# Performance work log

Hardware: AMD Instinct MI355X
Metric: run time of the kernel (lower is better)

## Reference

```python
import jax, jax.numpy as jnp
import numpy as np

B, N, D, H, S = 2, 1024, 1024, 16, 4
DH = D // H  # dim_head = 64


def setup_inputs() -> dict:
    key = jax.random.key(0)
    ks = jax.random.split(key, 7)
    w = lambda k, shape: jax.random.normal(k, shape, dtype=jnp.float32) * 0.02
    return {
        "x": jax.random.normal(ks[0], (B, N, D), dtype=jnp.float32),
        "Wq": w(ks[1], (S, D, D)),
        "Wk": w(ks[2], (S, D, D)),
        "Wv": w(ks[3], (S, D, D)),
        "Wg": w(ks[4], (S, D)),
        "bg": jnp.zeros((S,), jnp.float32),
        "Wo": w(ks[5], (D, D)),
        "bo": jnp.zeros((D,), jnp.float32),
        "hyp_w": jnp.ones((S,), jnp.float32),
        "temperature": jnp.float32(1.0),
    }


def reference(x, Wq, Wk, Wv, Wg, bg, Wo, bo, hyp_w, temperature):
    # Training branch of EnhancedUncertaintyAttention, all S samples batched.
    b, n, d = x.shape
    scale = DH ** -0.5
    temp = jnp.clip(temperature, 0.1, 10.0)

    # coherence gate on mean-pooled tokens: [b, S]
    coh = jax.nn.sigmoid(x.mean(axis=1) @ Wg.T + bg)

    def proj(W):  # torch Linear: x @ W.T ; W: [S, out, in] -> [s,b,h,n,dh]
        y = jnp.einsum('bnd,sed->sbne', x, W)
        return y.reshape(S, b, n, H, DH).transpose(0, 1, 3, 2, 4)

    q, k, v = proj(Wq), proj(Wk), proj(Wv)

    dots = jnp.einsum('sbhid,sbhjd->sbhij', q, k) * scale
    attn = jax.nn.softmax(dots / temp, axis=-1)            # [S,b,h,n,n]
    out = jnp.einsum('sbhij,sbhjd->sbhid', attn, v)        # [S,b,h,n,dh]
    out = out.transpose(0, 1, 3, 2, 4).reshape(S, b, n, d) # [S,b,n,d]
    out = out * coh.T[:, :, None, None]                    # per-sample gate

    gw = jax.nn.softmax(hyp_w / temp)                      # hypothesis weights [S]
    combined = jnp.einsum('s,sbnd->bnd', gw, out)
    combined_attn = jnp.einsum('s,sbhij->bhij', gw, attn)

    y = combined @ Wo.T + bo  # to_out; dropout p treated as 0 (deterministic)
    return y, combined_attn.mean(axis=1)
```

## Files before the change

kernel.cpp:

```cpp
#include <hip/hip_runtime.h>
#include <hip/hip_bf16.h>

typedef __attribute__((ext_vector_type(8))) short s16x8;
typedef __attribute__((ext_vector_type(4))) float f32x4;

#define MAT2M 2097152
#define NPAD 72
#define PPAD 72

__device__ __forceinline__ unsigned short f2bf(float f) {
  union { float f; unsigned u; } c; c.f = f;
  unsigned u = c.u;
  unsigned r = (u + 0x7fffu + ((u >> 16) & 1u)) >> 16;
  return (unsigned short)r;
}

__device__ __forceinline__ unsigned pk2bf(float a, float b) {
  union { __hip_bfloat162 h; unsigned u; } c;
  c.h = __float22bfloat162_rn(make_float2(a, b));
  return c.u;
}

__device__ __forceinline__ void async16(const unsigned short* g, unsigned short* l) {
  __builtin_amdgcn_global_load_lds(
      (const __attribute__((address_space(1))) unsigned int*)g,
      (__attribute__((address_space(3))) unsigned int*)l, 16, 0, 0);
}

__global__ __launch_bounds__(256) void k_cvt(const float* __restrict__ in,
                                             unsigned short* __restrict__ out, int n) {
  int i = (blockIdx.x * 256 + threadIdx.x) * 4;
  if (i < n) {
    float4 v = *(const float4*)&in[i];
    ushort4 o;
    o.x = f2bf(v.x); o.y = f2bf(v.y); o.z = f2bf(v.z); o.w = f2bf(v.w);
    *(ushort4*)&out[i] = o;
  }
}

__global__ __launch_bounds__(256) void k_meanx(const float* __restrict__ x,
                                               float* __restrict__ meanx) {
  int col = blockIdx.x * 256 + threadIdx.x;
  int b = col >> 10, d = col & 1023;
  int n0 = blockIdx.y * 64;
  float s = 0.f;
  for (int n = 0; n < 64; ++n)
    s += x[(size_t)b * 1048576 + (size_t)(n0 + n) * 1024 + d];
  atomicAdd(&meanx[col], s * (1.f / 1024.f));
}

__global__ __launch_bounds__(256) void k_prep(const float* __restrict__ meanx,
                                              const float* __restrict__ Wg,
                                              const float* __restrict__ bg,
                                              const float* __restrict__ hyp,
                                              const float* __restrict__ temp_p,
                                              float* __restrict__ prep) {
  int tid = threadIdx.x;
  int p = tid >> 5, c = tid & 31;
  int s = p >> 1, b = p & 1;
  float partial = 0.f;
  for (int d = c; d < 1024; d += 32)
    partial += meanx[b * 1024 + d] * Wg[s * 1024 + d];
#pragma unroll
  for (int m = 16; m >= 1; m >>= 1) partial += __shfl_xor(partial, m, 64);
  if (c == 0) {
    float coh = 1.f / (1.f + __expf(-(partial + bg[s])));
    prep[4 + s * 2 + b] = coh;
  }
  if (tid == 0) {
    float t = temp_p[0];
    t = fminf(fmaxf(t, 0.1f), 10.f);
    float it = 1.f / t;
    float e0 = hyp[0] * it, e1 = hyp[1] * it, e2 = hyp[2] * it, e3 = hyp[3] * it;
    float mx = fmaxf(fmaxf(e0, e1), fmaxf(e2, e3));
    float x0 = __expf(e0 - mx), x1 = __expf(e1 - mx), x2 = __expf(e2 - mx), x3 = __expf(e3 - mx);
    float inv = 1.f / (x0 + x1 + x2 + x3);
    prep[0] = x0 * inv; prep[1] = x1 * inv; prep[2] = x2 * inv; prep[3] = x3 * inv;
    prep[12] = 0.125f * it * 1.44269504f;
  }
}

__global__ __launch_bounds__(256) void gemm_qkv(
    const unsigned short* __restrict__ xb,
    const unsigned short* __restrict__ wqb,
    const unsigned short* __restrict__ wkb,
    const unsigned short* __restrict__ wvb,
    const float* __restrict__ prep,
    unsigned short* __restrict__ qk,
    unsigned short* __restrict__ vt) {
  __shared__ __align__(16) unsigned short As[128 * 32];
  __shared__ __align__(16) unsigned short Bs[128 * 32];
  const int tid = threadIdx.x;
  const int wid = tid >> 6, ln = tid & 63, lq = ln >> 4, lc = ln & 15;
  const int wr = wid >> 1, wc = wid & 1;
  const int z = blockIdx.z, proj = z >> 2, s = z & 3;
  const unsigned short* Bmat =
      (proj == 0 ? wqb : (proj == 1 ? wkb : wvb)) + (size_t)s * 1048576;
  const int n0 = blockIdx.x * 128, m0 = blockIdx.y * 128;
  const int srow = wid * 32 + (ln >> 2);
  const int scol = (ln & 3) * 8;
  const int lds0 = wid * 1024 + ln * 8;

  f32x4 acc[4][4];
#pragma unroll
  for (int a = 0; a < 4; ++a)
#pragma unroll
    for (int b4 = 0; b4 < 4; ++b4) acc[a][b4] = (f32x4){0.f, 0.f, 0.f, 0.f};

  for (int kt = 0; kt < 32; ++kt) {
    const int k0 = kt * 32;
    __syncthreads();
    async16(&xb[(size_t)(m0 + srow) * 1024 + k0 + scol], &As[lds0]);
    async16(&xb[(size_t)(m0 + srow + 16) * 1024 + k0 + scol], &As[lds0 + 512]);
    async16(&Bmat[(size_t)(n0 + srow) * 1024 + k0 + scol], &Bs[lds0]);
    async16(&Bmat[(size_t)(n0 + srow + 16) * 1024 + k0 + scol], &Bs[lds0 + 512]);
    __syncthreads();
    s16x8 af[4], bf[4];
#pragma unroll
    for (int a = 0; a < 4; ++a)
      af[a] = *(const s16x8*)&As[(wr * 64 + a * 16 + lc) * 32 + lq * 8];
#pragma unroll
    for (int b4 = 0; b4 < 4; ++b4)
      bf[b4] = *(const s16x8*)&Bs[(wc * 64 + b4 * 16 + lc) * 32 + lq * 8];
#pragma unroll
    for (int a = 0; a < 4; ++a)
#pragma unroll
      for (int b4 = 0; b4 < 4; ++b4)
        acc[a][b4] = __builtin_amdgcn_mfma_f32_16x16x32_bf16(af[a], bf[b4], acc[a][b4], 0, 0, 0);
  }

  const float mulv = (proj == 1) ? prep[12] : 1.0f;
  if (z < 8) {
    unsigned short* C = qk + (size_t)z * MAT2M;
#pragma unroll
    for (int a = 0; a < 4; ++a) {
      int row0 = m0 + wr * 64 + a * 16 + lq * 4;
#pragma unroll
      for (int b4 = 0; b4 < 4; ++b4) {
        int col = n0 + wc * 64 + b4 * 16 + lc;
#pragma unroll
        for (int r = 0; r < 4; ++r)
          C[(size_t)(row0 + r) * 1024 + col] = f2bf(acc[a][b4][r] * mulv);
      }
    }
  } else {
#pragma unroll
    for (int a = 0; a < 4; ++a) {
      int row0 = m0 + wr * 64 + a * 16 + lq * 4;
      int bb = row0 >> 10, ii = row0 & 1023;
#pragma unroll
      for (int b4 = 0; b4 < 4; ++b4) {
        int col = n0 + wc * 64 + b4 * 16 + lc;
        int head = col >> 6, dh = col & 63;
        ushort4 pk;
        pk.x = f2bf(acc[a][b4][0]); pk.y = f2bf(acc[a][b4][1]);
        pk.z = f2bf(acc[a][b4][2]); pk.w = f2bf(acc[a][b4][3]);
        *(ushort4*)&vt[(((size_t)((s * 2 + bb) * 16 + head)) << 16) + dh * 1024 + ii] = pk;
      }
    }
  }
}

__device__ __forceinline__ void stage64(const unsigned short* __restrict__ g,
                                        unsigned short* l, int tid) {
  const int r1 = tid >> 3;
  const int c8 = (tid & 7) * 8;
  *(float4*)&l[r1 * NPAD + c8] = *(const float4*)&g[(size_t)r1 * 1024 + c8];
  *(float4*)&l[(r1 + 32) * NPAD + c8] = *(const float4*)&g[(size_t)(r1 + 32) * 1024 + c8];
}

__global__ __launch_bounds__(256) void att_o(
    const unsigned short* __restrict__ qk,
    const unsigned short* __restrict__ vt,
    float* __restrict__ o_s,
    float* __restrict__ linv_ws) {
  __shared__ __align__(16) unsigned short ks[64 * NPAD];
  __shared__ __align__(16) unsigned short vts[64 * NPAD];
  __shared__ __align__(16) unsigned short PB[8 * 16 * PPAD];

  const int tid = threadIdx.x;
  const int wid = tid >> 6, ln = tid & 63, lq = ln >> 4, lc = ln & 15;
  const int i0 = blockIdx.x * 128;
  const int h = blockIdx.y;
  const int sb = blockIdx.z, s = sb >> 1, b = sb & 1;

  const unsigned short* Qg =
      qk + (size_t)s * MAT2M + (size_t)(b * 1024 + i0 + wid * 32) * 1024 + h * 64;
  const unsigned short* Kg = qk + (size_t)(4 + s) * MAT2M + (size_t)b * 1048576 + h * 64;
  const unsigned short* Vtg = vt + (((size_t)(sb * 16 + h)) << 16);

  s16x8 qf[2][2];
#pragma unroll
  for (int g = 0; g < 2; ++g)
#pragma unroll
    for (int kc = 0; kc < 2; ++kc)
      qf[g][kc] = *(const s16x8*)&Qg[(size_t)(g * 16 + lc) * 1024 + kc * 32 + lq * 8];

  f32x4 oaccT[2][4];
#pragma unroll
  for (int g = 0; g < 2; ++g)
#pragma unroll
    for (int db = 0; db < 4; ++db) oaccT[g][db] = (f32x4){0.f, 0.f, 0.f, 0.f};
  float lsum[2] = {0.f, 0.f};
  unsigned short* PBw = PB + wid * 2 * 16 * PPAD;

  for (int jt = 0; jt < 16; ++jt) {
    __syncthreads();
    stage64(Kg + (size_t)jt * 64 * 1024, ks, tid);
    stage64(Vtg + jt * 64, vts, tid);
    __syncthreads();

    f32x4 st[2][4];
#pragma unroll
    for (int g = 0; g < 2; ++g)
#pragma unroll
      for (int jb = 0; jb < 4; ++jb) st[g][jb] = (f32x4){0.f, 0.f, 0.f, 0.f};
#pragma unroll
    for (int jb = 0; jb < 4; ++jb)
#pragma unroll
      for (int kc = 0; kc < 2; ++kc) {
        s16x8 kf = *(const s16x8*)&ks[(jb * 16 + lc) * NPAD + kc * 32 + lq * 8];
        st[0][jb] = __builtin_amdgcn_mfma_f32_16x16x32_bf16(kf, qf[0][kc], st[0][jb], 0, 0, 0);
        st[1][jb] = __builtin_amdgcn_mfma_f32_16x16x32_bf16(kf, qf[1][kc], st[1][jb], 0, 0, 0);
      }

#pragma unroll
    for (int g = 0; g < 2; ++g)
#pragma unroll
      for (int jb = 0; jb < 4; ++jb) {
        float p0 = __builtin_amdgcn_exp2f(st[g][jb][0]);
        float p1 = __builtin_amdgcn_exp2f(st[g][jb][1]);
        float p2 = __builtin_amdgcn_exp2f(st[g][jb][2]);
        float p3 = __builtin_amdgcn_exp2f(st[g][jb][3]);
        lsum[g] += (p0 + p1) + (p2 + p3);
        uint2 pv;
        pv.x = pk2bf(p0, p1);
        pv.y = pk2bf(p2, p3);
        *(uint2*)&PBw[(g * 16 + lc) * PPAD + jb * 16 + lq * 4] = pv;
      }

#pragma unroll
    for (int kc = 0; kc < 2; ++kc) {
      s16x8 pf0 = *(const s16x8*)&PBw[lc * PPAD + kc * 32 + lq * 8];
      s16x8 pf1 = *(const s16x8*)&PBw[(16 + lc) * PPAD + kc * 32 + lq * 8];
#pragma unroll
      for (int db = 0; db < 4; ++db) {
        s16x8 vf = *(const s16x8*)&vts[(db * 16 + lc) * NPAD + kc * 32 + lq * 8];
        oaccT[0][db] = __builtin_amdgcn_mfma_f32_16x16x32_bf16(vf, pf0, oaccT[0][db], 0, 0, 0);
        oaccT[1][db] = __builtin_amdgcn_mfma_f32_16x16x32_bf16(vf, pf1, oaccT[1][db], 0, 0, 0);
      }
    }
  }

  float invl[2];
#pragma unroll
  for (int g = 0; g < 2; ++g) {
    lsum[g] += __shfl_xor(lsum[g], 16, 64);
    lsum[g] += __shfl_xor(lsum[g], 32, 64);
    invl[g] = 1.f / lsum[g];
  }
  if (lq == 0) {
    int base = (sb * 16 + h) * 1024 + i0 + wid * 32 + lc;
    linv_ws[base] = invl[0];
    linv_ws[base + 16] = invl[1];
  }

#pragma unroll
  for (int g = 0; g < 2; ++g) {
    int i = i0 + wid * 32 + g * 16 + lc;
    float* orow = o_s + (size_t)s * MAT2M + (size_t)(b * 1024 + i) * 1024 + h * 64;
#pragma unroll
    for (int db = 0; db < 4; ++db) {
      f32x4 o = oaccT[g][db] * invl[g];
      *(f32x4*)&orow[db * 16 + lq * 4] = o;
    }
  }
}

__global__ __launch_bounds__(256) void att_p(
    const unsigned short* __restrict__ qk,
    const float* __restrict__ prep,
    const float* __restrict__ linv_ws,
    float* __restrict__ out1) {
  __shared__ __align__(16) unsigned short qs[128 * NPAD];
  __shared__ __align__(16) unsigned short ks[64 * NPAD];
  const int tid = threadIdx.x;
  const int wid = tid >> 6, ln = tid & 63, lq = ln >> 4, lc = ln & 15;
  const int j0 = blockIdx.x * 64;
  const int i0 = blockIdx.y * 128;
  const int b = blockIdx.z;

  f32x4 psum[2][4];
#pragma unroll
  for (int g = 0; g < 2; ++g)
#pragma unroll
    for (int jb = 0; jb < 4; ++jb) psum[g][jb] = (f32x4){0.f, 0.f, 0.f, 0.f};

  for (int s = 0; s < 4; ++s) {
    const float wgt = prep[s] * (1.f / 16.f);
    const unsigned short* Qb = qk + (size_t)s * MAT2M + (size_t)(b * 1024 + i0) * 1024;
    const unsigned short* Kb = qk + (size_t)(4 + s) * MAT2M + (size_t)(b * 1024 + j0) * 1024;
    for (int h = 0; h < 16; ++h) {
      __syncthreads();
      stage64(Qb + h * 64, qs, tid);
      stage64(Qb + (size_t)64 * 1024 + h * 64, qs + 64 * NPAD, tid);
      stage64(Kb + h * 64, ks, tid);
      __syncthreads();
      s16x8 qf[2][2];
#pragma unroll
      for (int g = 0; g < 2; ++g)
#pragma unroll
        for (int kc = 0; kc < 2; ++kc)
          qf[g][kc] = *(const s16x8*)&qs[(wid * 32 + g * 16 + lc) * NPAD + kc * 32 + lq * 8];
      float ilr[2];
#pragma unroll
      for (int g = 0; g < 2; ++g)
        ilr[g] = wgt * linv_ws[((s * 2 + b) * 16 + h) * 1024 + i0 + wid * 32 + g * 16 + lc];
      f32x4 st[2][4];
#pragma unroll
      for (int g = 0; g < 2; ++g)
#pragma unroll
        for (int jb = 0; jb < 4; ++jb) st[g][jb] = (f32x4){0.f, 0.f, 0.f, 0.f};
#pragma unroll
      for (int jb = 0; jb < 4; ++jb)
#pragma unroll
        for (int kc = 0; kc < 2; ++kc) {
          s16x8 kf = *(const s16x8*)&ks[(jb * 16 + lc) * NPAD + kc * 32 + lq * 8];
          st[0][jb] = __builtin_amdgcn_mfma_f32_16x16x32_bf16(kf, qf[0][kc], st[0][jb], 0, 0, 0);
          st[1][jb] = __builtin_amdgcn_mfma_f32_16x16x32_bf16(kf, qf[1][kc], st[1][jb], 0, 0, 0);
        }
#pragma unroll
      for (int g = 0; g < 2; ++g)
#pragma unroll
        for (int jb = 0; jb < 4; ++jb)
#pragma unroll
          for (int r = 0; r < 4; ++r)
            psum[g][jb][r] += __builtin_amdgcn_exp2f(st[g][jb][r]) * ilr[g];
    }
  }
#pragma unroll
  for (int g = 0; g < 2; ++g) {
    int i = i0 + wid * 32 + g * 16 + lc;
    float* row = out1 + (size_t)b * 1048576 + (size_t)i * 1024;
#pragma unroll
    for (int jb = 0; jb < 4; ++jb)
      *(f32x4*)&row[j0 + jb * 16 + lq * 4] = psum[g][jb];
  }
}

__global__ __launch_bounds__(256) void k_combine(const float* __restrict__ o_s,
                                                 const float* __restrict__ prep,
                                                 unsigned short* __restrict__ comb) {
  size_t base = (size_t)(blockIdx.x * 256 + threadIdx.x) * 4;
  int m = (int)(base >> 10);
  int b = m >> 10;
  float w0 = prep[0] * prep[4 + 0 * 2 + b];
  float w1 = prep[1] * prep[4 + 1 * 2 + b];
  float w2 = prep[2] * prep[4 + 2 * 2 + b];
  float w3 = prep[3] * prep[4 + 3 * 2 + b];
  float4 v0 = *(const float4*)&o_s[base];
  float4 v1 = *(const float4*)&o_s[(size_t)MAT2M + base];
  float4 v2 = *(const float4*)&o_s[(size_t)2 * MAT2M + base];
  float4 v3 = *(const float4*)&o_s[(size_t)3 * MAT2M + base];
  float4 a;
  a.x = w0 * v0.x + w1 * v1.x + w2 * v2.x + w3 * v3.x;
  a.y = w0 * v0.y + w1 * v1.y + w2 * v2.y + w3 * v3.y;
  a.z = w0 * v0.z + w1 * v1.z + w2 * v2.z + w3 * v3.z;
  a.w = w0 * v0.w + w1 * v1.w + w2 * v2.w + w3 * v3.w;
  ushort4 o;
  o.x = f2bf(a.x); o.y = f2bf(a.y); o.z = f2bf(a.z); o.w = f2bf(a.w);
  *(ushort4*)&comb[base] = o;
}

__global__ __launch_bounds__(256) void gemm_out(
    const unsigned short* __restrict__ Amat,
    const unsigned short* __restrict__ Bmat,
    const float* __restrict__ bias,
    float* __restrict__ y) {
  __shared__ __align__(16) unsigned short As[128 * 32];
  __shared__ __align__(16) unsigned short Bs[128 * 32];
  const int tid = threadIdx.x;
  const int wid = tid >> 6, ln = tid & 63, lq = ln >> 4, lc = ln & 15;
  const int wr = wid >> 1, wc = wid & 1;
  const int n0 = blockIdx.x * 128, m0 = blockIdx.y * 128;
  const int srow = wid * 32 + (ln >> 2);
  const int scol = (ln & 3) * 8;
  const int lds0 = wid * 1024 + ln * 8;

  f32x4 acc[4][4];
#pragma unroll
  for (int a = 0; a < 4; ++a)
#pragma unroll
    for (int b4 = 0; b4 < 4; ++b4) acc[a][b4] = (f32x4){0.f, 0.f, 0.f, 0.f};

  for (int kt = 0; kt < 32; ++kt) {
    const int k0 = kt * 32;
    __syncthreads();
    async16(&Amat[(size_t)(m0 + srow) * 1024 + k0 + scol], &As[lds0]);
    async16(&Amat[(size_t)(m0 + srow + 16) * 1024 + k0 + scol], &As[lds0 + 512]);
    async16(&Bmat[(size_t)(n0 + srow) * 1024 + k0 + scol], &Bs[lds0]);
    async16(&Bmat[(size_t)(n0 + srow + 16) * 1024 + k0 + scol], &Bs[lds0 + 512]);
    __syncthreads();
    s16x8 af[4], bf[4];
#pragma unroll
    for (int a = 0; a < 4; ++a)
      af[a] = *(const s16x8*)&As[(wr * 64 + a * 16 + lc) * 32 + lq * 8];
#pragma unroll
    for (int b4 = 0; b4 < 4; ++b4)
      bf[b4] = *(const s16x8*)&Bs[(wc * 64 + b4 * 16 + lc) * 32 + lq * 8];
#pragma unroll
    for (int a = 0; a < 4; ++a)
#pragma unroll
      for (int b4 = 0; b4 < 4; ++b4)
        acc[a][b4] = __builtin_amdgcn_mfma_f32_16x16x32_bf16(af[a], bf[b4], acc[a][b4], 0, 0, 0);
  }

#pragma unroll
  for (int a = 0; a < 4; ++a) {
    int row0 = m0 + wr * 64 + a * 16 + lq * 4;
#pragma unroll
    for (int b4 = 0; b4 < 4; ++b4) {
      int col = n0 + wc * 64 + b4 * 16 + lc;
      float bv = bias[col];
#pragma unroll
      for (int r = 0; r < 4; ++r)
        y[(size_t)(row0 + r) * 1024 + col] = acc[a][b4][r] + bv;
    }
  }
}

extern "C" void kernel_launch(void* const* d_in, const int* in_sizes, int n_in,
                              void* d_out, int out_size, void* d_ws, size_t ws_size,
                              hipStream_t stream) {
  const float* x    = (const float*)d_in[0];
  const float* Wq   = (const float*)d_in[1];
  const float* Wk   = (const float*)d_in[2];
  const float* Wv   = (const float*)d_in[3];
  const float* Wg   = (const float*)d_in[4];
  const float* bg   = (const float*)d_in[5];
  const float* Wo   = (const float*)d_in[6];
  const float* bo   = (const float*)d_in[7];
  const float* hyp  = (const float*)d_in[8];
  const float* temp = (const float*)d_in[9];

  float* y = (float*)d_out;
  float* out1 = y + MAT2M;

  char* w = (char*)d_ws;
  size_t off = 0;
  auto alloc = [&](size_t bytes) { void* p = w + off; off += (bytes + 255) & ~(size_t)255; return p; };
  unsigned short* xb   = (unsigned short*)alloc((size_t)MAT2M * 2);
  unsigned short* wqb  = (unsigned short*)alloc((size_t)4 * 1048576 * 2);
  unsigned short* wkb  = (unsigned short*)alloc((size_t)4 * 1048576 * 2);
  unsigned short* wvb  = (unsigned short*)alloc((size_t)4 * 1048576 * 2);
  unsigned short* wob  = (unsigned short*)alloc((size_t)1048576 * 2);
  unsigned short* qk   = (unsigned short*)alloc((size_t)8 * MAT2M * 2);
  unsigned short* vt   = (unsigned short*)alloc((size_t)4 * MAT2M * 2);
  float* o_s   = (float*)alloc((size_t)4 * MAT2M * 4);
  unsigned short* comb = (unsigned short*)alloc((size_t)MAT2M * 2);
  float* linv  = (float*)alloc((size_t)131072 * 4);
  float* meanx = (float*)alloc((size_t)2048 * 4);
  float* prep  = (float*)alloc((size_t)16 * 4);

  k_cvt<<<2048, 256, 0, stream>>>(x, xb, MAT2M);
  k_cvt<<<4096, 256, 0, stream>>>(Wq, wqb, 4 * 1048576);
  k_cvt<<<4096, 256, 0, stream>>>(Wk, wkb, 4 * 1048576);
  k_cvt<<<4096, 256, 0, stream>>>(Wv, wvb, 4 * 1048576);
  k_cvt<<<1024, 256, 0, stream>>>(Wo, wob, 1048576);

  hipMemsetAsync(meanx, 0, 2048 * sizeof(float), stream);
  k_meanx<<<dim3(8, 16), 256, 0, stream>>>(x, meanx);
  k_prep<<<1, 256, 0, stream>>>(meanx, Wg, bg, hyp, temp, prep);

  gemm_qkv<<<dim3(8, 16, 12), 256, 0, stream>>>(xb, wqb, wkb, wvb, prep, qk, vt);

  att_o<<<dim3(8, 16, 8), 256, 0, stream>>>(qk, vt, o_s, linv);
  att_p<<<dim3(16, 8, 2), 256, 0, stream>>>(qk, prep, linv, out1);

  k_combine<<<2048, 256, 0, stream>>>(o_s, prep, comb);
  gemm_out<<<dim3(8, 16, 1), 256, 0, stream>>>(comb, wob, bo, y);
}
```

Before: 373.2 us.

## Widen GEMM K-tiles with swizzled LDS, drop attention LDS staging, split att_p by sample

Both GEMMs now load 64-wide K tiles into an XOR-swizzled LDS layout, which halves the barrier count and avoids bank conflicts. The attention kernels drop their shared-memory staging of K and V and read MFMA fragments straight from global memory. att_p is split across samples (grid z 2→8) for more parallelism, and its partial results are merged with atomics into a pre-zeroed output. The per-sample attention output is stored in bf16 instead of fp32 to halve combine traffic, and the three weight conversions are fused into one launch. The risks are uncoalesced direct global fragment loads, float-atomic contention and ordering nondeterminism in the averaged attention map, and extra bf16 rounding.

New measurement: 539.0 us. 1.44x slower.

```diff
diff --git a/kernel.cpp b/kernel.cpp
--- a/kernel.cpp
+++ b/kernel.cpp
@@ -5,7 +5,6 @@
 typedef __attribute__((ext_vector_type(4))) float f32x4;
 
 #define MAT2M 2097152
-#define NPAD 72
 #define PPAD 72
 
 __device__ __forceinline__ unsigned short f2bf(float f) {
@@ -19,6 +18,10 @@
   union { __hip_bfloat162 h; unsigned u; } c;
   c.h = __float22bfloat162_rn(make_float2(a, b));
   return c.u;
+}
+
+__device__ __forceinline__ float bf2f(unsigned short u) {
+  union { unsigned u; float f; } c; c.u = ((unsigned)u) << 16; return c.f;
 }
 
 __device__ __forceinline__ void async16(const unsigned short* g, unsigned short* l) {
@@ -36,6 +39,21 @@
     o.x = f2bf(v.x); o.y = f2bf(v.y); o.z = f2bf(v.z); o.w = f2bf(v.w);
     *(ushort4*)&out[i] = o;
   }
+}
+
+__global__ __launch_bounds__(256) void k_cvt3(const float* __restrict__ a,
+                                              const float* __restrict__ b,
+                                              const float* __restrict__ c,
+                                              unsigned short* __restrict__ oa,
+                                              unsigned short* __restrict__ ob,
+                                              unsigned short* __restrict__ oc) {
+  const float* in = blockIdx.y == 0 ? a : (blockIdx.y == 1 ? b : c);
+  unsigned short* out = blockIdx.y == 0 ? oa : (blockIdx.y == 1 ? ob : oc);
+  int i = (blockIdx.x * 256 + threadIdx.x) * 4;
+  float4 v = *(const float4*)&in[i];
+  ushort4 o;
+  o.x = f2bf(v.x); o.y = f2bf(v.y); o.z = f2bf(v.z); o.w = f2bf(v.w);
+  *(ushort4*)&out[i] = o;
 }
 
 __global__ __launch_bounds__(256) void k_meanx(const float* __restrict__ x,
@@ -88,8 +106,8 @@
     const float* __restrict__ prep,
     unsigned short* __restrict__ qk,
     unsigned short* __restrict__ vt) {
-  __shared__ __align__(16) unsigned short As[128 * 32];
-  __shared__ __align__(16) unsigned short Bs[128 * 32];
+  __shared__ __align__(16) unsigned short As[128 * 64];
+  __shared__ __align__(16) unsigned short Bs[128 * 64];
   const int tid = threadIdx.x;
   const int wid = tid >> 6, ln = tid & 63, lq = ln >> 4, lc = ln & 15;
   const int wr = wid >> 1, wc = wid & 1;
@@ -97,9 +115,9 @@
   const unsigned short* Bmat =
       (proj == 0 ? wqb : (proj == 1 ? wkb : wvb)) + (size_t)s * 1048576;
   const int n0 = blockIdx.x * 128, m0 = blockIdx.y * 128;
-  const int srow = wid * 32 + (ln >> 2);
-  const int scol = (ln & 3) * 8;
-  const int lds0 = wid * 1024 + ln * 8;
+  const int sr = wid * 8 + (ln >> 3);
+  const int sc = (((ln & 7) ^ ((ln >> 3) & 7))) * 8;
+  const int ldsoff = wid * 512 + ln * 8;
 
   f32x4 acc[4][4];
 #pragma unroll
@@ -107,26 +125,31 @@
 #pragma unroll
     for (int b4 = 0; b4 < 4; ++b4) acc[a][b4] = (f32x4){0.f, 0.f, 0.f, 0.f};
 
-  for (int kt = 0; kt < 32; ++kt) {
-    const int k0 = kt * 32;
+  for (int kt = 0; kt < 16; ++kt) {
+    const int k0 = kt * 64;
     __syncthreads();
-    async16(&xb[(size_t)(m0 + srow) * 1024 + k0 + scol], &As[lds0]);
-    async16(&xb[(size_t)(m0 + srow + 16) * 1024 + k0 + scol], &As[lds0 + 512]);
-    async16(&Bmat[(size_t)(n0 + srow) * 1024 + k0 + scol], &Bs[lds0]);
-    async16(&Bmat[(size_t)(n0 + srow + 16) * 1024 + k0 + scol], &Bs[lds0 + 512]);
+#pragma unroll
+    for (int c = 0; c < 4; ++c) {
+      async16(&xb[(size_t)(m0 + c * 32 + sr) * 1024 + k0 + sc], &As[c * 2048 + ldsoff]);
+      async16(&Bmat[(size_t)(n0 + c * 32 + sr) * 1024 + k0 + sc], &Bs[c * 2048 + ldsoff]);
+    }
     __syncthreads();
-    s16x8 af[4], bf[4];
-#pragma unroll
-    for (int a = 0; a < 4; ++a)
-      af[a] = *(const s16x8*)&As[(wr * 64 + a * 16 + lc) * 32 + lq * 8];
-#pragma unroll
-    for (int b4 = 0; b4 < 4; ++b4)
-      bf[b4] = *(const s16x8*)&Bs[(wc * 64 + b4 * 16 + lc) * 32 + lq * 8];
-#pragma unroll
-    for (int a = 0; a < 4; ++a)
+#pragma unroll
+    for (int kc = 0; kc < 2; ++kc) {
+      const int slot = ((kc * 4 + lq) ^ (lc & 7)) * 8;
+      s16x8 af[4], bf[4];
+#pragma unroll
+      for (int a = 0; a < 4; ++a)
+        af[a] = *(const s16x8*)&As[(wr * 64 + a * 16 + lc) * 64 + slot];
 #pragma unroll
       for (int b4 = 0; b4 < 4; ++b4)
-        acc[a][b4] = __builtin_amdgcn_mfma_f32_16x16x32_bf16(af[a], bf[b4], acc[a][b4], 0, 0, 0);
+        bf[b4] = *(const s16x8*)&Bs[(wc * 64 + b4 * 16 + lc) * 64 + slot];
+#pragma unroll
+      for (int a = 0; a < 4; ++a)
+#pragma unroll
+        for (int b4 = 0; b4 < 4; ++b4)
+          acc[a][b4] = __builtin_amdgcn_mfma_f32_16x16x32_bf16(af[a], bf[b4], acc[a][b4], 0, 0, 0);
+    }
   }
 
   const float mulv = (proj == 1) ? prep[12] : 1.0f;
@@ -152,30 +175,20 @@
       for (int b4 = 0; b4 < 4; ++b4) {
         int col = n0 + wc * 64 + b4 * 16 + lc;
         int head = col >> 6, dh = col & 63;
-        ushort4 pk;
-        pk.x = f2bf(acc[a][b4][0]); pk.y = f2bf(acc[a][b4][1]);
-        pk.z = f2bf(acc[a][b4][2]); pk.w = f2bf(acc[a][b4][3]);
-        *(ushort4*)&vt[(((size_t)((s * 2 + bb) * 16 + head)) << 16) + dh * 1024 + ii] = pk;
-      }
-    }
-  }
-}
-
-__device__ __forceinline__ void stage64(const unsigned short* __restrict__ g,
-                                        unsigned short* l, int tid) {
-  const int r1 = tid >> 3;
-  const int c8 = (tid & 7) * 8;
-  *(float4*)&l[r1 * NPAD + c8] = *(const float4*)&g[(size_t)r1 * 1024 + c8];
-  *(float4*)&l[(r1 + 32) * NPAD + c8] = *(const float4*)&g[(size_t)(r1 + 32) * 1024 + c8];
+        uint2 pk;
+        pk.x = pk2bf(acc[a][b4][0], acc[a][b4][1]);
+        pk.y = pk2bf(acc[a][b4][2], acc[a][b4][3]);
+        *(uint2*)&vt[(((size_t)((s * 2 + bb) * 16 + head)) << 16) + dh * 1024 + ii] = pk;
+      }
+    }
+  }
 }
 
 __global__ __launch_bounds__(256) void att_o(
     const unsigned short* __restrict__ qk,
     const unsigned short* __restrict__ vt,
-    float* __restrict__ o_s,
+    unsigned short* __restrict__ o_sb,
     float* __restrict__ linv_ws) {
-  __shared__ __align__(16) unsigned short ks[64 * NPAD];
-  __shared__ __align__(16) unsigned short vts[64 * NPAD];
   __shared__ __align__(16) unsigned short PB[8 * 16 * PPAD];
 
   const int tid = threadIdx.x;
@@ -205,10 +218,8 @@
   unsigned short* PBw = PB + wid * 2 * 16 * PPAD;
 
   for (int jt = 0; jt < 16; ++jt) {
-    __syncthreads();
-    stage64(Kg + (size_t)jt * 64 * 1024, ks, tid);
-    stage64(Vtg + jt * 64, vts, tid);
-    __syncthreads();
+    const unsigned short* Kj = Kg + (size_t)jt * 64 * 1024;
+    const unsigned short* Vj = Vtg + jt * 64;
 
     f32x4 st[2][4];
 #pragma unroll
@@ -219,7 +230,7 @@
     for (int jb = 0; jb < 4; ++jb)
 #pragma unroll
       for (int kc = 0; kc < 2; ++kc) {
-        s16x8 kf = *(const s16x8*)&ks[(jb * 16 + lc) * NPAD + kc * 32 + lq * 8];
+        s16x8 kf = *(const s16x8*)&Kj[(size_t)(jb * 16 + lc) * 1024 + kc * 32 + lq * 8];
         st[0][jb] = __builtin_amdgcn_mfma_f32_16x16x32_bf16(kf, qf[0][kc], st[0][jb], 0, 0, 0);
         st[1][jb] = __builtin_amdgcn_mfma_f32_16x16x32_bf16(kf, qf[1][kc], st[1][jb], 0, 0, 0);
       }
@@ -245,7 +256,7 @@
       s16x8 pf1 = *(const s16x8*)&PBw[(16 + lc) * PPAD + kc * 32 + lq * 8];
 #pragma unroll
       for (int db = 0; db < 4; ++db) {
-        s16x8 vf = *(const s16x8*)&vts[(db * 16 + lc) * NPAD + kc * 32 + lq * 8];
+        s16x8 vf = *(const s16x8*)&Vj[(size_t)(db * 16 + lc) * 1024 + kc * 32 + lq * 8];
         oaccT[0][db] = __builtin_amdgcn_mfma_f32_16x16x32_bf16(vf, pf0, oaccT[0][db], 0, 0, 0);
         oaccT[1][db] = __builtin_amdgcn_mfma_f32_16x16x32_bf16(vf, pf1, oaccT[1][db], 0, 0, 0);
       }
@@ -268,11 +279,15 @@
 #pragma unroll
   for (int g = 0; g < 2; ++g) {
     int i = i0 + wid * 32 + g * 16 + lc;
-    float* orow = o_s + (size_t)s * MAT2M + (size_t)(b * 1024 + i) * 1024 + h * 64;
+    unsigned short* orow =
+        o_sb + (size_t)s * MAT2M + (size_t)(b * 1024 + i) * 1024 + h * 64;
 #pragma unroll
     for (int db = 0; db < 4; ++db) {
       f32x4 o = oaccT[g][db] * invl[g];
-      *(f32x4*)&orow[db * 16 + lq * 4] = o;
+      uint2 pv;
+      pv.x = pk2bf(o[0], o[1]);
+      pv.y = pk2bf(o[2], o[3]);
+      *(uint2*)&orow[db * 16 + lq * 4] = pv;
     }
   }
 }
@@ -282,13 +297,16 @@
     const float* __restrict__ prep,
     const float* __restrict__ linv_ws,
     float* __restrict__ out1) {
-  __shared__ __align__(16) unsigned short qs[128 * NPAD];
-  __shared__ __align__(16) unsigned short ks[64 * NPAD];
   const int tid = threadIdx.x;
   const int wid = tid >> 6, ln = tid & 63, lq = ln >> 4, lc = ln & 15;
   const int j0 = blockIdx.x * 64;
   const int i0 = blockIdx.y * 128;
-  const int b = blockIdx.z;
+  const int z = blockIdx.z, s = z >> 1, b = z & 1;
+  const float wgt = prep[s] * (1.f / 16.f);
+
+  const unsigned short* Qb =
+      qk + (size_t)s * MAT2M + (size_t)(b * 1024 + i0 + wid * 32) * 1024;
+  const unsigned short* Kb = qk + (size_t)(4 + s) * MAT2M + (size_t)(b * 1024 + j0) * 1024;
 
   f32x4 psum[2][4];
 #pragma unroll
@@ -296,59 +314,53 @@
 #pragma unroll
     for (int jb = 0; jb < 4; ++jb) psum[g][jb] = (f32x4){0.f, 0.f, 0.f, 0.f};
 
-  for (int s = 0; s < 4; ++s) {
-    const float wgt = prep[s] * (1.f / 16.f);
-    const unsigned short* Qb = qk + (size_t)s * MAT2M + (size_t)(b * 1024 + i0) * 1024;
-    const unsigned short* Kb = qk + (size_t)(4 + s) * MAT2M + (size_t)(b * 1024 + j0) * 1024;
-    for (int h = 0; h < 16; ++h) {
-      __syncthreads();
-      stage64(Qb + h * 64, qs, tid);
-      stage64(Qb + (size_t)64 * 1024 + h * 64, qs + 64 * NPAD, tid);
-      stage64(Kb + h * 64, ks, tid);
-      __syncthreads();
-      s16x8 qf[2][2];
-#pragma unroll
-      for (int g = 0; g < 2; ++g)
-#pragma unroll
-        for (int kc = 0; kc < 2; ++kc)
-          qf[g][kc] = *(const s16x8*)&qs[(wid * 32 + g * 16 + lc) * NPAD + kc * 32 + lq * 8];
-      float ilr[2];
-#pragma unroll
-      for (int g = 0; g < 2; ++g)
-        ilr[g] = wgt * linv_ws[((s * 2 + b) * 16 + h) * 1024 + i0 + wid * 32 + g * 16 + lc];
-      f32x4 st[2][4];
-#pragma unroll
-      for (int g = 0; g < 2; ++g)
-#pragma unroll
-        for (int jb = 0; jb < 4; ++jb) st[g][jb] = (f32x4){0.f, 0.f, 0.f, 0.f};
+  for (int h = 0; h < 16; ++h) {
+    const int hoff = h * 64;
+    s16x8 qf[2][2];
+#pragma unroll
+    for (int g = 0; g < 2; ++g)
+#pragma unroll
+      for (int kc = 0; kc < 2; ++kc)
+        qf[g][kc] = *(const s16x8*)&Qb[(size_t)(g * 16 + lc) * 1024 + hoff + kc * 32 + lq * 8];
+    float ilr[2];
+#pragma unroll
+    for (int g = 0; g < 2; ++g)
+      ilr[g] = wgt * linv_ws[(z * 16 + h) * 1024 + i0 + wid * 32 + g * 16 + lc];
+    f32x4 st[2][4];
+#pragma unroll
+    for (int g = 0; g < 2; ++g)
+#pragma unroll
+      for (int jb = 0; jb < 4; ++jb) st[g][jb] = (f32x4){0.f, 0.f, 0.f, 0.f};
+#pragma unroll
+    for (int jb = 0; jb < 4; ++jb)
+#pragma unroll
+      for (int kc = 0; kc < 2; ++kc) {
+        s16x8 kf = *(const s16x8*)&Kb[(size_t)(jb * 16 + lc) * 1024 + hoff + kc * 32 + lq * 8];
+        st[0][jb] = __builtin_amdgcn_mfma_f32_16x16x32_bf16(kf, qf[0][kc], st[0][jb], 0, 0, 0);
+        st[1][jb] = __builtin_amdgcn_mfma_f32_16x16x32_bf16(kf, qf[1][kc], st[1][jb], 0, 0, 0);
+      }
+#pragma unroll
+    for (int g = 0; g < 2; ++g)
 #pragma unroll
       for (int jb = 0; jb < 4; ++jb)
 #pragma unroll
-        for (int kc = 0; kc < 2; ++kc) {
-          s16x8 kf = *(const s16x8*)&ks[(jb * 16 + lc) * NPAD + kc * 32 + lq * 8];
-          st[0][jb] = __builtin_amdgcn_mfma_f32_16x16x32_bf16(kf, qf[0][kc], st[0][jb], 0, 0, 0);
-          st[1][jb] = __builtin_amdgcn_mfma_f32_16x16x32_bf16(kf, qf[1][kc], st[1][jb], 0, 0, 0);
-        }
-#pragma unroll
-      for (int g = 0; g < 2; ++g)
-#pragma unroll
-        for (int jb = 0; jb < 4; ++jb)
-#pragma unroll
-          for (int r = 0; r < 4; ++r)
-            psum[g][jb][r] += __builtin_amdgcn_exp2f(st[g][jb][r]) * ilr[g];
-    }
-  }
+        for (int r = 0; r < 4; ++r)
+          psum[g][jb][r] += __builtin_amdgcn_exp2f(st[g][jb][r]) * ilr[g];
+  }
+
 #pragma unroll
   for (int g = 0; g < 2; ++g) {
     int i = i0 + wid * 32 + g * 16 + lc;
     float* row = out1 + (size_t)b * 1048576 + (size_t)i * 1024;
 #pragma unroll
     for (int jb = 0; jb < 4; ++jb)
-      *(f32x4*)&row[j0 + jb * 16 + lq * 4] = psum[g][jb];
-  }
-}
-
-__global__ __launch_bounds__(256) void k_combine(const float* __restrict__ o_s,
+#pragma unroll
+      for (int r = 0; r < 4; ++r)
+        atomicAdd(&row[j0 + jb * 16 + lq * 4 + r], psum[g][jb][r]);
+  }
+}
+
+__global__ __launch_bounds__(256) void k_combine(const unsigned short* __restrict__ o_sb,
                                                  const float* __restrict__ prep,
                                                  unsigned short* __restrict__ comb) {
   size_t base = (size_t)(blockIdx.x * 256 + threadIdx.x) * 4;
@@ -358,18 +370,18 @@
   float w1 = prep[1] * prep[4 + 1 * 2 + b];
   float w2 = prep[2] * prep[4 + 2 * 2 + b];
   float w3 = prep[3] * prep[4 + 3 * 2 + b];
-  float4 v0 = *(const float4*)&o_s[base];
-  float4 v1 = *(const float4*)&o_s[(size_t)MAT2M + base];
-  float4 v2 = *(const float4*)&o_s[(size_t)2 * MAT2M + base];
-  float4 v3 = *(const float4*)&o_s[(size_t)3 * MAT2M + base];
-  float4 a;
-  a.x = w0 * v0.x + w1 * v1.x + w2 * v2.x + w3 * v3.x;
-  a.y = w0 * v0.y + w1 * v1.y + w2 * v2.y + w3 * v3.y;
-  a.z = w0 * v0.z + w1 * v1.z + w2 * v2.z + w3 * v3.z;
-  a.w = w0 * v0.w + w1 * v1.w + w2 * v2.w + w3 * v3.w;
-  ushort4 o;
-  o.x = f2bf(a.x); o.y = f2bf(a.y); o.z = f2bf(a.z); o.w = f2bf(a.w);
-  *(ushort4*)&comb[base] = o;
+  ushort4 v0 = *(const ushort4*)&o_sb[base];
+  ushort4 v1 = *(const ushort4*)&o_sb[(size_t)MAT2M + base];
+  ushort4 v2 = *(const ushort4*)&o_sb[(size_t)2 * MAT2M + base];
+  ushort4 v3 = *(const ushort4*)&o_sb[(size_t)3 * MAT2M + base];
+  float ax = w0 * bf2f(v0.x) + w1 * bf2f(v1.x) + w2 * bf2f(v2.x) + w3 * bf2f(v3.x);
+  float ay = w0 * bf2f(v0.y) + w1 * bf2f(v1.y) + w2 * bf2f(v2.y) + w3 * bf2f(v3.y);
+  float az = w0 * bf2f(v0.z) + w1 * bf2f(v1.z) + w2 * bf2f(v2.z) + w3 * bf2f(v3.z);
+  float aw = w0 * bf2f(v0.w) + w1 * bf2f(v1.w) + w2 * bf2f(v2.w) + w3 * bf2f(v3.w);
+  uint2 o;
+  o.x = pk2bf(ax, ay);
+  o.y = pk2bf(az, aw);
+  *(uint2*)&comb[base] = o;
 }
 
 __global__ __launch_bounds__(256) void gemm_out(
@@ -377,15 +389,15 @@
     const unsigned short* __restrict__ Bmat,
     const float* __restrict__ bias,
     float* __restrict__ y) {
-  __shared__ __align__(16) unsigned short As[128 * 32];
-  __shared__ __align__(16) unsigned short Bs[128 * 32];
+  __shared__ __align__(16) unsigned short As[128 * 64];
+  __shared__ __align__(16) unsigned short Bs[128 * 64];
   const int tid = threadIdx.x;
   const int wid = tid >> 6, ln = tid & 63, lq = ln >> 4, lc = ln & 15;
   const int wr = wid >> 1, wc = wid & 1;
   const int n0 = blockIdx.x * 128, m0 = blockIdx.y * 128;
-  const int srow = wid * 32 + (ln >> 2);
-  const int scol = (ln & 3) * 8;
-  const int lds0 = wid * 1024 + ln * 8;
+  const int sr = wid * 8 + (ln >> 3);
+  const int sc = (((ln & 7) ^ ((ln >> 3) & 7))) * 8;
+  const int ldsoff = wid * 512 + ln * 8;
 
   f32x4 acc[4][4];
 #pragma unroll
@@ -393,26 +405,31 @@
 #pragma unroll
     for (int b4 = 0; b4 < 4; ++b4) acc[a][b4] = (f32x4){0.f, 0.f, 0.f, 0.f};
 
-  for (int kt = 0; kt < 32; ++kt) {
-    const int k0 = kt * 32;
+  for (int kt = 0; kt < 16; ++kt) {
+    const int k0 = kt * 64;
     __syncthreads();
-    async16(&Amat[(size_t)(m0 + srow) * 1024 + k0 + scol], &As[lds0]);
-    async16(&Amat[(size_t)(m0 + srow + 16) * 1024 + k0 + scol], &As[lds0 + 512]);
-    async16(&Bmat[(size_t)(n0 + srow) * 1024 + k0 + scol], &Bs[lds0]);
-    async16(&Bmat[(size_t)(n0 + srow + 16) * 1024 + k0 + scol], &Bs[lds0 + 512]);
+#pragma unroll
+    for (int c = 0; c < 4; ++c) {
+      async16(&Amat[(size_t)(m0 + c * 32 + sr) * 1024 + k0 + sc], &As[c * 2048 + ldsoff]);
+      async16(&Bmat[(size_t)(n0 + c * 32 + sr) * 1024 + k0 + sc], &Bs[c * 2048 + ldsoff]);
+    }
     __syncthreads();
-    s16x8 af[4], bf[4];
-#pragma unroll
-    for (int a = 0; a < 4; ++a)
-      af[a] = *(const s16x8*)&As[(wr * 64 + a * 16 + lc) * 32 + lq * 8];
-#pragma unroll
-    for (int b4 = 0; b4 < 4; ++b4)
-      bf[b4] = *(const s16x8*)&Bs[(wc * 64 + b4 * 16 + lc) * 32 + lq * 8];
-#pragma unroll
-    for (int a = 0; a < 4; ++a)
+#pragma unroll
+    for (int kc = 0; kc < 2; ++kc) {
+      const int slot = ((kc * 4 + lq) ^ (lc & 7)) * 8;
+      s16x8 af[4], bf[4];
+#pragma unroll
+      for (int a = 0; a < 4; ++a)
+        af[a] = *(const s16x8*)&As[(wr * 64 + a * 16 + lc) * 64 + slot];
 #pragma unroll
       for (int b4 = 0; b4 < 4; ++b4)
-        acc[a][b4] = __builtin_amdgcn_mfma_f32_16x16x32_bf16(af[a], bf[b4], acc[a][b4], 0, 0, 0);
+        bf[b4] = *(const s16x8*)&Bs[(wc * 64 + b4 * 16 + lc) * 64 + slot];
+#pragma unroll
+      for (int a = 0; a < 4; ++a)
+#pragma unroll
+        for (int b4 = 0; b4 < 4; ++b4)
+          acc[a][b4] = __builtin_amdgcn_mfma_f32_16x16x32_bf16(af[a], bf[b4], acc[a][b4], 0, 0, 0);
+    }
   }
 
 #pragma unroll
@@ -456,27 +473,26 @@
   unsigned short* wob  = (unsigned short*)alloc((size_t)1048576 * 2);
   unsigned short* qk   = (unsigned short*)alloc((size_t)8 * MAT2M * 2);
   unsigned short* vt   = (unsigned short*)alloc((size_t)4 * MAT2M * 2);
-  float* o_s   = (float*)alloc((size_t)4 * MAT2M * 4);
+  unsigned short* o_sb = (unsigned short*)alloc((size_t)4 * MAT2M * 2);
   unsigned short* comb = (unsigned short*)alloc((size_t)MAT2M * 2);
   float* linv  = (float*)alloc((size_t)131072 * 4);
   float* meanx = (float*)alloc((size_t)2048 * 4);
   float* prep  = (float*)alloc((size_t)16 * 4);
 
   k_cvt<<<2048, 256, 0, stream>>>(x, xb, MAT2M);
-  k_cvt<<<4096, 256, 0, stream>>>(Wq, wqb, 4 * 1048576);
-  k_cvt<<<4096, 256, 0, stream>>>(Wk, wkb, 4 * 1048576);
-  k_cvt<<<4096, 256, 0, stream>>>(Wv, wvb, 4 * 1048576);
+  k_cvt3<<<dim3(4096, 3), 256, 0, stream>>>(Wq, Wk, Wv, wqb, wkb, wvb);
   k_cvt<<<1024, 256, 0, stream>>>(Wo, wob, 1048576);
 
   hipMemsetAsync(meanx, 0, 2048 * sizeof(float), stream);
+  hipMemsetAsync(out1, 0, (size_t)MAT2M * sizeof(float), stream);
   k_meanx<<<dim3(8, 16), 256, 0, stream>>>(x, meanx);
   k_prep<<<1, 256, 0, stream>>>(meanx, Wg, bg, hyp, temp, prep);
 
   gemm_qkv<<<dim3(8, 16, 12), 256, 0, stream>>>(xb, wqb, wkb, wvb, prep, qk, vt);
 
-  att_o<<<dim3(8, 16, 8), 256, 0, stream>>>(qk, vt, o_s, linv);
-  att_p<<<dim3(16, 8, 2), 256, 0, stream>>>(qk, prep, linv, out1);
-
-  k_combine<<<2048, 256, 0, stream>>>(o_s, prep, comb);
+  att_o<<<dim3(8, 16, 8), 256, 0, stream>>>(qk, vt, o_sb, linv);
+  att_p<<<dim3(16, 8, 8), 256, 0, stream>>>(qk, prep, linv, out1);
+
+  k_combine<<<2048, 256, 0, stream>>>(o_sb, prep, comb);
   gemm_out<<<dim3(8, 16, 1), 256, 0, stream>>>(comb, wob, bo, y);
 }
```
